# Kernel optimization log

Measured on AMD Instinct MI355X. Metric: run time of the kernel, lower is better.

## Reference

```python
import jax, jax.numpy as jnp
import numpy as np

B, L, D, H = 16, 512, 1024, 16
DH = D // H
NEG = -1e9  # stands in for -inf mask fill (same softmax result, grad-safe)


def setup_inputs() -> dict:
    key = jax.random.key(0)
    ks = jax.random.split(key, 8)
    x = jax.random.normal(ks[0], (B, L, D), dtype=jnp.float32)
    mask = jnp.ones((B, L), dtype=jnp.int64)
    qmask = jax.random.randint(ks[1], (B, L), 0, 9).astype(jnp.int64)
    # qkv_linear: Linear(D, 4D, bias=False); store as [D, 4D] so y = x @ Wqkv
    Wqkv = jax.random.normal(ks[2], (D, 4 * D), dtype=jnp.float32) / np.sqrt(D)
    # fc: Linear(D, D) with bias; store as [D, D] so y = x @ Wfc + bfc
    Wfc = jax.random.normal(ks[3], (D, D), dtype=jnp.float32) / np.sqrt(D)
    bfc = jnp.zeros((D,), dtype=jnp.float32)
    shift = jnp.abs(jax.random.normal(ks[4], (1,), dtype=jnp.float32)) + 0.001
    bias_p = -jnp.abs(jax.random.normal(ks[5], (1,), dtype=jnp.float32))
    return {"x": x, "mask": mask, "qmask": qmask, "Wqkv": Wqkv,
            "Wfc": Wfc, "bfc": bfc, "shift": shift, "bias_p": bias_p,
            "use_Gaussian": 1}


def reference(x, mask, qmask, Wqkv, Wfc, bfc, shift, bias_p, use_Gaussian):
    b, l, d = x.shape
    qkv = x @ Wqkv                                  # [B, L, 4D]
    q, k1, k2, v = jnp.split(qkv, 4, axis=-1)
    q = q.reshape(b, l, H, DH)                      # [B, L, H, dh]
    k1 = k1.reshape(b, l, H, DH)
    k2 = k2.reshape(b, l, H, DH)
    v = v.reshape(b, l, H, DH)

    attn_self = jnp.einsum('bqhd,bkhd->bhqk', q, k1)    # [B, H, L, L]
    attn_others = jnp.einsum('bqhd,bkhd->bhqk', q, k2)  # [B, H, L, L]

    same = (qmask[:, :, None] == qmask[:, None, :])[:, None]  # [B, 1, L, L]
    attn = jnp.where(same, attn_self, attn_others)  # scale == 1 (scale=False)

    key_valid = (mask != 0)[:, None, None, :]       # [B, 1, 1, L]
    attn = jnp.where(key_valid, attn, NEG)

    if use_Gaussian:
        idx = jnp.arange(l, dtype=jnp.float32)
        sq_dist = (idx[:, None] - idx[None, :]) ** 2        # [L, L]
        dis = -(shift[0] * sq_dist + bias_p[0])
        attn = attn + dis[None, None]

    attn = jax.nn.softmax(attn, axis=-1)            # dropout: eval mode (no-op)
    out = jnp.einsum('bhqk,bkhd->bqhd', attn, v).reshape(b, l, d)
    return out @ Wfc + bfc
```

## Files before the change

kernel.cpp:

```cpp
#include <hip/hip_runtime.h>
#include <hip/hip_bf16.h>

#define B_  16
#define L_  512
#define D_  1024
#define H_  16
#define DH_ 64
#define NEG_ (-1e9f)
#define QB_ 64
#define KB_ 64
#define LDP 72

#define GK  1024
#define NT  32

typedef unsigned short ushort_t;
typedef __attribute__((ext_vector_type(8))) short bf16x8;
typedef __attribute__((ext_vector_type(4))) float f32x4;

__device__ __forceinline__ ushort_t f2bf(float f) {
    unsigned u = __float_as_uint(f);
    u += 0x7FFFu + ((u >> 16) & 1u);
    return (ushort_t)(u >> 16);
}
__device__ __forceinline__ unsigned packbf(float a, float b) {
    return (unsigned)f2bf(a) | ((unsigned)f2bf(b) << 16);
}

__device__ __forceinline__ void gload_lds16(const void* g, void* l) {
    __builtin_amdgcn_global_load_lds(
        (const __attribute__((address_space(1))) void*)g,
        (__attribute__((address_space(3))) void*)l, 16, 0, 0);
}

__global__ __launch_bounds__(256) void conv_f32_bf16(const float* __restrict__ in,
                                                     ushort_t* __restrict__ out, int n) {
    const int i = (blockIdx.x * 256 + threadIdx.x) * 4;
    if (i < n) {
        const float4 v = *(const float4*)&in[i];
        ushort4 o;
        o.x = f2bf(v.x); o.y = f2bf(v.y); o.z = f2bf(v.z); o.w = f2bf(v.w);
        *(ushort4*)&out[i] = o;
    }
}

__global__ __launch_bounds__(256) void transpose_f32_bf16(const float* __restrict__ in,
                                                          ushort_t* __restrict__ out,
                                                          int R, int C) {
    __shared__ float tile[32][33];
    const int t  = threadIdx.x;
    const int r0 = blockIdx.y * 32, c0 = blockIdx.x * 32;
    const int tr = t >> 3;
    const int tc = (t & 7) * 4;
    const float4 v = *(const float4*)&in[(size_t)(r0 + tr) * C + c0 + tc];
    tile[tr][tc + 0] = v.x;
    tile[tr][tc + 1] = v.y;
    tile[tr][tc + 2] = v.z;
    tile[tr][tc + 3] = v.w;
    __syncthreads();
    ushort4 o;
    o.x = f2bf(tile[tc + 0][tr]);
    o.y = f2bf(tile[tc + 1][tr]);
    o.z = f2bf(tile[tc + 2][tr]);
    o.w = f2bf(tile[tc + 3][tr]);
    *(ushort4*)&out[(size_t)(c0 + tr) * R + r0 + tc] = o;
}

template <bool OUT_BF16>
__global__ __launch_bounds__(256) void gemm_bf16_mfma(const ushort_t* __restrict__ A,
                                                      const ushort_t* __restrict__ Bt,
                                                      const float* __restrict__ bias,
                                                      void* __restrict__ C,
                                                      int M, int N, int K) {
    __shared__ __align__(16) ushort_t As[128 * 64];
    __shared__ __align__(16) ushort_t Bs[128 * 64];

    const int t    = threadIdx.x;
    const int wave = t >> 6;
    const int lane = t & 63;
    const int m0   = blockIdx.y * 128;
    const int n0   = blockIdx.x * 128;
    const int wr   = wave >> 1;
    const int wc   = wave & 1;

    const int lrow = lane >> 3;
    const int lcol = (lane & 7) * 8;

    f32x4 acc[4][4] = {};

    for (int k0 = 0; k0 < K; k0 += 64) {
        #pragma unroll
        for (int i = 0; i < 4; ++i) {
            const int row = wave * 32 + i * 8;
            gload_lds16(A + (size_t)(m0 + row + lrow) * K + k0 + lcol,
                        As + (size_t)row * 64);
            gload_lds16(Bt + (size_t)(n0 + row + lrow) * K + k0 + lcol,
                        Bs + (size_t)row * 64);
        }
        __syncthreads();

        #pragma unroll
        for (int ks = 0; ks < 2; ++ks) {
            const int kb = ks * 32 + (lane >> 4) * 8;
            bf16x8 af[4], bfr[4];
            #pragma unroll
            for (int m = 0; m < 4; ++m)
                af[m] = *(const bf16x8*)&As[(wr * 64 + m * 16 + (lane & 15)) * 64 + kb];
            #pragma unroll
            for (int n = 0; n < 4; ++n)
                bfr[n] = *(const bf16x8*)&Bs[(wc * 64 + n * 16 + (lane & 15)) * 64 + kb];
            #pragma unroll
            for (int m = 0; m < 4; ++m)
                #pragma unroll
                for (int n = 0; n < 4; ++n)
                    acc[m][n] = __builtin_amdgcn_mfma_f32_16x16x32_bf16(
                        af[m], bfr[n], acc[m][n], 0, 0, 0);
        }
        __syncthreads();
    }

    #pragma unroll
    for (int m = 0; m < 4; ++m) {
        #pragma unroll
        for (int n = 0; n < 4; ++n) {
            const int col = n0 + wc * 64 + n * 16 + (lane & 15);
            const float bv = OUT_BF16 ? 0.f : bias[col];
            #pragma unroll
            for (int i = 0; i < 4; ++i) {
                const int row = m0 + wr * 64 + m * 16 + (lane >> 4) * 4 + i;
                const float v = acc[m][n][i];
                if (OUT_BF16)
                    ((ushort_t*)C)[(size_t)row * N + col] = f2bf(v);
                else
                    ((float*)C)[(size_t)row * N + col] = v + bv;
            }
        }
    }
}

__device__ __forceinline__ bf16x8 frag_ld(const ushort_t* tile, int row, int lhi) {
    const int slot = lhi ^ ((row >> 1) & 3);
    return *(const bf16x8*)&tile[row * 32 + (slot << 3)];
}

__global__ __launch_bounds__(512, 2) void gemm256_8p(const ushort_t* __restrict__ A,
                                                     const ushort_t* __restrict__ Bt,
                                                     ushort_t* __restrict__ C,
                                                     int nbn, int N) {
    extern __shared__ __align__(16) ushort_t lds[];

    const int t    = threadIdx.x;
    const int wave = t >> 6;
    const int lane = t & 63;
    const int wr   = wave >> 2;
    const int wc   = wave & 3;
    const int lhi  = lane >> 4;
    const int llo  = lane & 15;
    const int srow  = lane >> 2;
    const int sslot = (lane & 3) ^ ((lane >> 3) & 3);

    const int cpx = gridDim.x >> 3;
    const int bid = blockIdx.x;
    const int swz = (bid & 7) * cpx + (bid >> 3);
    const int m0  = (swz / nbn) * 256;
    const int n0  = (swz % nbn) * 256;

    #define STAGE_H(mat, gptr, grow0, kt, half)                                         \
        gload_lds16((gptr) + (size_t)((grow0) + (half) * 128 + (wave << 4) + srow) * GK \
                        + (kt) * 32 + (sslot << 3),                                     \
                    lds + ((((kt) & 3) * 2 + (mat)) * 8192                              \
                           + ((half) * 128 + (wave << 4)) * 32))

    f32x4 acc[8][4] = {};

    STAGE_H(0, A,  m0, 0, 0); STAGE_H(0, A,  m0, 0, 1);
    STAGE_H(1, Bt, n0, 0, 0); STAGE_H(1, Bt, n0, 0, 1);
    STAGE_H(0, A,  m0, 1, 0); STAGE_H(0, A,  m0, 1, 1);
    STAGE_H(1, Bt, n0, 1, 0); STAGE_H(1, Bt, n0, 1, 1);
    asm volatile("s_waitcnt vmcnt(4)" ::: "memory");
    __builtin_amdgcn_s_barrier();

    for (int kt = 0; kt < NT; ++kt) {
        const ushort_t* At  = lds + ((kt & 3) * 2 + 0) * 8192;
        const ushort_t* Bti = lds + ((kt & 3) * 2 + 1) * 8192;

        bf16x8 afr[4], bfr[4];

        #pragma unroll
        for (int n = 0; n < 4; ++n)
            bfr[n] = frag_ld(Bti, wc * 64 + n * 16 + llo, lhi);
        #pragma unroll
        for (int mi = 0; mi < 4; ++mi)
            afr[mi] = frag_ld(At, wr * 128 + mi * 16 + llo, lhi);
        if (kt + 2 < NT) {
            STAGE_H(0, A, m0, kt + 2, 0);
            STAGE_H(0, A, m0, kt + 2, 1);
        }
        __builtin_amdgcn_s_setprio(1);
        #pragma unroll
        for (int mi = 0; mi < 4; ++mi)
            #pragma unroll
            for (int n = 0; n < 4; ++n)
                acc[mi][n] = __builtin_amdgcn_mfma_f32_16x16x32_bf16(
                    afr[mi], bfr[n], acc[mi][n], 0, 0, 0);
        __builtin_amdgcn_s_setprio(0);

        #pragma unroll
        for (int mi = 0; mi < 4; ++mi)
            afr[mi] = frag_ld(At, wr * 128 + (mi + 4) * 16 + llo, lhi);
        if (kt + 2 < NT) {
            STAGE_H(1, Bt, n0, kt + 2, 0);
            STAGE_H(1, Bt, n0, kt + 2, 1);
        }
        __builtin_amdgcn_s_setprio(1);
        #pragma unroll
        for (int mi = 0; mi < 4; ++mi)
            #pragma unroll
            for (int n = 0; n < 4; ++n)
                acc[mi + 4][n] = __builtin_amdgcn_mfma_f32_16x16x32_bf16(
                    afr[mi], bfr[n], acc[mi + 4][n], 0, 0, 0);
        __builtin_amdgcn_s_setprio(0);

        if (kt + 2 < NT)      { asm volatile("s_waitcnt vmcnt(4)" ::: "memory"); }
        else if (kt + 1 < NT) { asm volatile("s_waitcnt vmcnt(0)" ::: "memory"); }
        __builtin_amdgcn_s_barrier();
    }
    #undef STAGE_H

    #pragma unroll
    for (int mi = 0; mi < 8; ++mi) {
        #pragma unroll
        for (int n = 0; n < 4; ++n) {
            const int col = n0 + wc * 64 + n * 16 + llo;
            #pragma unroll
            for (int i = 0; i < 4; ++i) {
                const int row = m0 + wr * 128 + mi * 16 + lhi * 4 + i;
                C[(size_t)row * N + col] = f2bf(acc[mi][n][i]);
            }
        }
    }
}

__global__ __launch_bounds__(256) void attn_mfma(const ushort_t* __restrict__ qkv,
                                                 const int* __restrict__ mask,
                                                 const int* __restrict__ qmask,
                                                 const float* __restrict__ shiftp,
                                                 const float* __restrict__ biasp,
                                                 const int* __restrict__ useg,
                                                 ushort_t* __restrict__ O) {
    __shared__ __align__(16) ushort_t K1s[KB_][LDP];
    __shared__ __align__(16) ushort_t K2s[KB_][LDP];
    __shared__ __align__(16) ushort_t Vt[DH_][LDP];
    __shared__ __align__(16) unsigned Ps32[QB_][36];
    __shared__ __align__(16) int      Ms[L_];

    const int t    = threadIdx.x;
    const int wave = t >> 6;
    const int lane = t & 63;
    const int lhi  = lane >> 4;
    const int llo  = lane & 15;

    const int orig = blockIdx.x;
    const int swz  = (orig & 7) * 256 + (orig >> 3);
    const int bh   = swz >> 3;
    const int qb   = swz & 7;
    const int b    = bh >> 4;
    const int h    = bh & 15;
    const int q0   = qb * QB_;

    const float shiftv = shiftp[0];
    const float biasv  = biasp[0];
    const int   useG   = useg[0];
    const size_t rowbase = (size_t)b * L_ * (4 * D_);
    const int    hoff    = h * DH_;

    {
        const int k = t;
        Ms[k]       = (qmask[b * L_ + k] << 1) | (mask[b * L_ + k] != 0 ? 1 : 0);
        Ms[k + 256] = (qmask[b * L_ + k + 256] << 1) | (mask[b * L_ + k + 256] != 0 ? 1 : 0);
    }

    const int gq = q0 + wave * 16 + llo;
    bf16x8 af_q[2];
    #pragma unroll
    for (int ks = 0; ks < 2; ++ks)
        af_q[ks] = *(const bf16x8*)&qkv[rowbase + (size_t)gq * (4 * D_) + hoff
                                        + ks * 32 + lhi * 8];
    const int qm_q = qmask[b * L_ + gq];

    int lo = 0, hi = (L_ / KB_) - 1;
    if (useG) {
        while (lo < hi) {
            const int k0 = lo * KB_;
            int dmin = (k0 > q0) ? (k0 - (q0 + KB_ - 1)) : (q0 - (k0 + KB_ - 1));
            if (dmin < 0) dmin = 0;
            if (shiftv * (float)dmin * (float)dmin > 240.f) ++lo; else break;
        }
        while (hi > lo) {
            const int k0 = hi * KB_;
            int dmin = (k0 > q0) ? (k0 - (q0 + KB_ - 1)) : (q0 - (k0 + KB_ - 1));
            if (dmin < 0) dmin = 0;
            if (shiftv * (float)dmin * (float)dmin > 240.f) --hi; else break;
        }
    }

    float m_run = -1e30f, l_run = 0.f;
    f32x4 acc_o[4] = {};

    const int srow8 = t >> 3;
    const int scol8 = (t & 7) * 8;
    const int vkv   = t & 63;
    const int vd0   = (t >> 6) * 8;

    uint4 pk1[2], pk2[2], pvv[2];

    #define ISSUE_KV(kt_) do {                                                          \
        const int k0_ = (kt_) * KB_;                                                    \
        _Pragma("unroll")                                                               \
        for (int it = 0; it < 2; ++it) {                                                \
            const int row = srow8 + it * 32;                                            \
            const size_t gb = rowbase + (size_t)(k0_ + row) * (4 * D_) + hoff + scol8;  \
            pk1[it] = *(const uint4*)&qkv[gb + D_];                                     \
            pk2[it] = *(const uint4*)&qkv[gb + 2 * D_];                                 \
            const int d_ = vd0 + it * 32;                                               \
            pvv[it] = *(const uint4*)&qkv[rowbase + (size_t)(k0_ + vkv) * (4 * D_)      \
                                          + 3 * D_ + hoff + d_];                        \
        }                                                                               \
    } while (0)

    ISSUE_KV(lo);

    for (int kt = lo; kt <= hi; ++kt) {
        const int k0 = kt * KB_;

        #pragma unroll
        for (int it = 0; it < 2; ++it) {
            const int row = srow8 + it * 32;
            *(uint4*)&K1s[row][scol8] = pk1[it];
            *(uint4*)&K2s[row][scol8] = pk2[it];
            const int d = vd0 + it * 32;
            const uint4 raw = pvv[it];
            Vt[d + 0][vkv] = (ushort_t)(raw.x & 0xFFFFu);
            Vt[d + 1][vkv] = (ushort_t)(raw.x >> 16);
            Vt[d + 2][vkv] = (ushort_t)(raw.y & 0xFFFFu);
            Vt[d + 3][vkv] = (ushort_t)(raw.y >> 16);
            Vt[d + 4][vkv] = (ushort_t)(raw.z & 0xFFFFu);
            Vt[d + 5][vkv] = (ushort_t)(raw.z >> 16);
            Vt[d + 6][vkv] = (ushort_t)(raw.w & 0xFFFFu);
            Vt[d + 7][vkv] = (ushort_t)(raw.w >> 16);
        }
        if (kt < hi) ISSUE_KV(kt + 1);
        __syncthreads();

        f32x4 s1[4], s2[4];
        #pragma unroll
        for (int n = 0; n < 4; ++n) { s1[n] = (f32x4){0,0,0,0}; s2[n] = (f32x4){0,0,0,0}; }
        #pragma unroll
        for (int ks = 0; ks < 2; ++ks) {
            const int kb = ks * 32 + lhi * 8;
            #pragma unroll
            for (int n = 0; n < 4; ++n) {
                const bf16x8 bk1 = *(const bf16x8*)&K1s[n * 16 + llo][kb];
                const bf16x8 bk2 = *(const bf16x8*)&K2s[n * 16 + llo][kb];
                s1[n] = __builtin_amdgcn_mfma_f32_16x16x32_bf16(bk1, af_q[ks], s1[n], 0, 0, 0);
                s2[n] = __builtin_amdgcn_mfma_f32_16x16x32_bf16(bk2, af_q[ks], s2[n], 0, 0, 0);
            }
        }

        float sv[4][4];
        float mx = -1e30f;
        #pragma unroll
        for (int n = 0; n < 4; ++n) {
            const int4 mc = *(const int4*)&Ms[k0 + n * 16 + lhi * 4];
            const int mci[4] = {mc.x, mc.y, mc.z, mc.w};
            #pragma unroll
            for (int i = 0; i < 4; ++i) {
                const int key = k0 + n * 16 + lhi * 4 + i;
                float x = ((mci[i] >> 1) == qm_q) ? s1[n][i] : s2[n][i];
                if (!(mci[i] & 1)) x = NEG_;
                if (useG) {
                    const float dq = (float)(gq - key);
                    x -= shiftv * dq * dq + biasv;
                }
                sv[n][i] = x;
                mx = fmaxf(mx, x);
            }
        }
        mx = fmaxf(mx, __shfl_xor(mx, 16));
        mx = fmaxf(mx, __shfl_xor(mx, 32));

        const float m_new = fmaxf(m_run, mx);
        const float scale = __expf(m_run - m_new);

        float p[4][4], ls = 0.f;
        #pragma unroll
        for (int n = 0; n < 4; ++n)
            #pragma unroll
            for (int i = 0; i < 4; ++i) {
                p[n][i] = __expf(sv[n][i] - m_new);
                ls += p[n][i];
            }
        ls += __shfl_xor(ls, 16);
        ls += __shfl_xor(ls, 32);
        l_run = l_run * scale + ls;
        m_run = m_new;

        #pragma unroll
        for (int n2 = 0; n2 < 4; ++n2) {
            acc_o[n2][0] *= scale; acc_o[n2][1] *= scale;
            acc_o[n2][2] *= scale; acc_o[n2][3] *= scale;
        }

        const int qrow = wave * 16 + llo;
        #pragma unroll
        for (int n = 0; n < 4; ++n) {
            uint2 w;
            w.x = packbf(p[n][0], p[n][1]);
            w.y = packbf(p[n][2], p[n][3]);
            *(uint2*)&Ps32[qrow][n * 8 + lhi * 2] = w;
        }

        #pragma unroll
        for (int ks = 0; ks < 2; ++ks) {
            const int kb = ks * 32 + lhi * 8;
            const bf16x8 bp = *(const bf16x8*)&Ps32[qrow][ks * 16 + lhi * 4];
            #pragma unroll
            for (int n2 = 0; n2 < 4; ++n2) {
                const bf16x8 av = *(const bf16x8*)&Vt[n2 * 16 + llo][kb];
                acc_o[n2] = __builtin_amdgcn_mfma_f32_16x16x32_bf16(av, bp, acc_o[n2], 0, 0, 0);
            }
        }
        __syncthreads();
    }
    #undef ISSUE_KV

    {
        const float inv = 1.f / l_run;
        const int qrow = wave * 16 + llo;
        #pragma unroll
        for (int n2 = 0; n2 < 4; ++n2) {
            uint2 w;
            w.x = packbf(acc_o[n2][0] * inv, acc_o[n2][1] * inv);
            w.y = packbf(acc_o[n2][2] * inv, acc_o[n2][3] * inv);
            *(uint2*)&Ps32[qrow][n2 * 8 + lhi * 2] = w;
        }
    }
    __syncthreads();
    {
        const int row = t >> 2;
        const int c4  = (t & 3) * 8;
        const uint4 a = *(const uint4*)&Ps32[row][c4];
        const uint4 b2 = *(const uint4*)&Ps32[row][c4 + 4];
        ushort_t* dst = &O[(size_t)(b * L_ + q0 + row) * D_ + hoff + c4 * 2];
        *(uint4*)dst       = a;
        *(uint4*)(dst + 8) = b2;
    }
}

extern "C" void kernel_launch(void* const* d_in, const int* in_sizes, int n_in,
                              void* d_out, int out_size, void* d_ws, size_t ws_size,
                              hipStream_t stream) {
    const float* x      = (const float*)d_in[0];
    const int*   mask   = (const int*)d_in[1];
    const int*   qmask  = (const int*)d_in[2];
    const float* Wqkv   = (const float*)d_in[3];
    const float* Wfc    = (const float*)d_in[4];
    const float* bfc    = (const float*)d_in[5];
    const float* shift  = (const float*)d_in[6];
    const float* bias_p = (const float*)d_in[7];
    const int*   useg   = (const int*)d_in[8];
    float*       out    = (float*)d_out;

    const int M  = B_ * L_;
    const int N1 = 4 * D_;

    ushort_t* qkv = (ushort_t*)d_ws;
    ushort_t* Obf = qkv + (size_t)M * N1;
    ushort_t* xbf = Obf + (size_t)M * D_;
    ushort_t* WqT = xbf + (size_t)M * D_;
    ushort_t* WfT = WqT + (size_t)N1 * D_;

    conv_f32_bf16<<<(M * D_) / 1024, 256, 0, stream>>>(x, xbf, M * D_);
    transpose_f32_bf16<<<dim3(N1 / 32, D_ / 32), 256, 0, stream>>>(Wqkv, WqT, D_, N1);
    transpose_f32_bf16<<<dim3(D_ / 32, D_ / 32), 256, 0, stream>>>(Wfc, WfT, D_, D_);

    gemm256_8p<<<dim3((M / 256) * (N1 / 256)), 512, 131072, stream>>>(
        xbf, WqT, qkv, N1 / 256, N1);

    attn_mfma<<<dim3((B_ * H_) * (L_ / QB_)), 256, 0, stream>>>(qkv, mask, qmask,
                                                                shift, bias_p, useg, Obf);

    gemm_bf16_mfma<false><<<dim3(D_ / 128, M / 128), 256, 0, stream>>>(
        Obf, WfT, bfc, out, M, D_, D_);
}
```

Before: 173.6 us.

## Fuse prep kernels, retile QKV GEMM to 128x256 with triple buffering, swizzle LDS

Merges the x conversion and both weight transposes into one launch, which cuts launch overhead. Replaces the 256x256, 4-stage QKV GEMM with a 128x256 tile that uses BK=64 and a 3-buffer pipeline, giving twice as many blocks for better CU fill. Adds an XOR swizzle to LDS staging in both GEMMs to reduce bank conflicts. In exchange, each block reuses less data and needs more LDS (147 KB per block), so occupancy may drop to one block per CU.

```diff
diff --git a/kernel.cpp b/kernel.cpp
--- a/kernel.cpp
+++ b/kernel.cpp
@@ -12,7 +12,7 @@
 #define LDP 72
 
 #define GK  1024
-#define NT  32
+#define NKT 16
 
 typedef unsigned short ushort_t;
 typedef __attribute__((ext_vector_type(8))) short bf16x8;
@@ -33,26 +33,36 @@
         (__attribute__((address_space(3))) void*)l, 16, 0, 0);
 }
 
-__global__ __launch_bounds__(256) void conv_f32_bf16(const float* __restrict__ in,
-                                                     ushort_t* __restrict__ out, int n) {
-    const int i = (blockIdx.x * 256 + threadIdx.x) * 4;
-    if (i < n) {
-        const float4 v = *(const float4*)&in[i];
+__global__ __launch_bounds__(256) void prep_all(const float* __restrict__ x,
+                                                const float* __restrict__ Wqkv,
+                                                const float* __restrict__ Wfc,
+                                                ushort_t* __restrict__ xbf,
+                                                ushort_t* __restrict__ WqT,
+                                                ushort_t* __restrict__ WfT) {
+    __shared__ float tile[32][33];
+    const int bid = blockIdx.x;
+    const int t   = threadIdx.x;
+
+    if (bid < 8192) {
+        const int i = (bid * 256 + t) * 4;
+        const float4 v = *(const float4*)&x[i];
         ushort4 o;
         o.x = f2bf(v.x); o.y = f2bf(v.y); o.z = f2bf(v.z); o.w = f2bf(v.w);
-        *(ushort4*)&out[i] = o;
-    }
-}
-
-__global__ __launch_bounds__(256) void transpose_f32_bf16(const float* __restrict__ in,
-                                                          ushort_t* __restrict__ out,
-                                                          int R, int C) {
-    __shared__ float tile[32][33];
-    const int t  = threadIdx.x;
-    const int r0 = blockIdx.y * 32, c0 = blockIdx.x * 32;
-    const int tr = t >> 3;
-    const int tc = (t & 7) * 4;
-    const float4 v = *(const float4*)&in[(size_t)(r0 + tr) * C + c0 + tc];
+        *(ushort4*)&xbf[i] = o;
+        return;
+    }
+    const float* src; ushort_t* dst; int C, gx, gy;
+    if (bid < 8192 + 4096) {
+        const int lb = bid - 8192;
+        src = Wqkv; dst = WqT; C = 4096; gx = lb & 127; gy = lb >> 7;
+    } else {
+        const int lb = bid - 12288;
+        src = Wfc;  dst = WfT; C = 1024; gx = lb & 31;  gy = lb >> 5;
+    }
+    const int R  = 1024;
+    const int r0 = gy * 32, c0 = gx * 32;
+    const int tr = t >> 3, tc = (t & 7) * 4;
+    const float4 v = *(const float4*)&src[(size_t)(r0 + tr) * C + c0 + tc];
     tile[tr][tc + 0] = v.x;
     tile[tr][tc + 1] = v.y;
     tile[tr][tc + 2] = v.z;
@@ -63,14 +73,13 @@
     o.y = f2bf(tile[tc + 1][tr]);
     o.z = f2bf(tile[tc + 2][tr]);
     o.w = f2bf(tile[tc + 3][tr]);
-    *(ushort4*)&out[(size_t)(c0 + tr) * R + r0 + tc] = o;
-}
-
-template <bool OUT_BF16>
+    *(ushort4*)&dst[(size_t)(c0 + tr) * R + r0 + tc] = o;
+}
+
 __global__ __launch_bounds__(256) void gemm_bf16_mfma(const ushort_t* __restrict__ A,
                                                       const ushort_t* __restrict__ Bt,
                                                       const float* __restrict__ bias,
-                                                      void* __restrict__ C,
+                                                      float* __restrict__ C,
                                                       int M, int N, int K) {
     __shared__ __align__(16) ushort_t As[128 * 64];
     __shared__ __align__(16) ushort_t Bs[128 * 64];
@@ -84,7 +93,9 @@
     const int wc   = wave & 1;
 
     const int lrow = lane >> 3;
-    const int lcol = (lane & 7) * 8;
+    const int ksl  = (lane & 7) ^ lrow;
+    const int llo  = lane & 15;
+    const int lhi  = lane >> 4;
 
     f32x4 acc[4][4] = {};
 
@@ -92,23 +103,26 @@
         #pragma unroll
         for (int i = 0; i < 4; ++i) {
             const int row = wave * 32 + i * 8;
-            gload_lds16(A + (size_t)(m0 + row + lrow) * K + k0 + lcol,
+            gload_lds16(A + (size_t)(m0 + row + lrow) * K + k0 + ksl * 8,
                         As + (size_t)row * 64);
-            gload_lds16(Bt + (size_t)(n0 + row + lrow) * K + k0 + lcol,
+            gload_lds16(Bt + (size_t)(n0 + row + lrow) * K + k0 + ksl * 8,
                         Bs + (size_t)row * 64);
         }
         __syncthreads();
 
         #pragma unroll
         for (int ks = 0; ks < 2; ++ks) {
-            const int kb = ks * 32 + (lane >> 4) * 8;
             bf16x8 af[4], bfr[4];
             #pragma unroll
-            for (int m = 0; m < 4; ++m)
-                af[m] = *(const bf16x8*)&As[(wr * 64 + m * 16 + (lane & 15)) * 64 + kb];
-            #pragma unroll
-            for (int n = 0; n < 4; ++n)
-                bfr[n] = *(const bf16x8*)&Bs[(wc * 64 + n * 16 + (lane & 15)) * 64 + kb];
+            for (int m = 0; m < 4; ++m) {
+                const int row = wr * 64 + m * 16 + llo;
+                af[m] = *(const bf16x8*)&As[row * 64 + (((ks * 4 + lhi) ^ (row & 7)) << 3)];
+            }
+            #pragma unroll
+            for (int n = 0; n < 4; ++n) {
+                const int row = wc * 64 + n * 16 + llo;
+                bfr[n] = *(const bf16x8*)&Bs[row * 64 + (((ks * 4 + lhi) ^ (row & 7)) << 3)];
+            }
             #pragma unroll
             for (int m = 0; m < 4; ++m)
                 #pragma unroll
@@ -123,30 +137,21 @@
     for (int m = 0; m < 4; ++m) {
         #pragma unroll
         for (int n = 0; n < 4; ++n) {
-            const int col = n0 + wc * 64 + n * 16 + (lane & 15);
-            const float bv = OUT_BF16 ? 0.f : bias[col];
+            const int col = n0 + wc * 64 + n * 16 + llo;
+            const float bv = bias[col];
             #pragma unroll
             for (int i = 0; i < 4; ++i) {
-                const int row = m0 + wr * 64 + m * 16 + (lane >> 4) * 4 + i;
-                const float v = acc[m][n][i];
-                if (OUT_BF16)
-                    ((ushort_t*)C)[(size_t)row * N + col] = f2bf(v);
-                else
-                    ((float*)C)[(size_t)row * N + col] = v + bv;
-            }
-        }
-    }
-}
-
-__device__ __forceinline__ bf16x8 frag_ld(const ushort_t* tile, int row, int lhi) {
-    const int slot = lhi ^ ((row >> 1) & 3);
-    return *(const bf16x8*)&tile[row * 32 + (slot << 3)];
-}
-
-__global__ __launch_bounds__(512, 2) void gemm256_8p(const ushort_t* __restrict__ A,
-                                                     const ushort_t* __restrict__ Bt,
-                                                     ushort_t* __restrict__ C,
-                                                     int nbn, int N) {
+                const int row = m0 + wr * 64 + m * 16 + lhi * 4 + i;
+                C[(size_t)row * N + col] = acc[m][n][i] + bv;
+            }
+        }
+    }
+}
+
+__global__ __launch_bounds__(512, 2) void gemm128x256(const ushort_t* __restrict__ A,
+                                                      const ushort_t* __restrict__ Bt,
+                                                      ushort_t* __restrict__ C,
+                                                      int nbn, int N) {
     extern __shared__ __align__(16) ushort_t lds[];
 
     const int t    = threadIdx.x;
@@ -156,85 +161,84 @@
     const int wc   = wave & 3;
     const int lhi  = lane >> 4;
     const int llo  = lane & 15;
-    const int srow  = lane >> 2;
-    const int sslot = (lane & 3) ^ ((lane >> 3) & 3);
 
     const int cpx = gridDim.x >> 3;
-    const int bid = blockIdx.x;
-    const int swz = (bid & 7) * cpx + (bid >> 3);
-    const int m0  = (swz / nbn) * 256;
+    const int swz = (blockIdx.x & 7) * cpx + (blockIdx.x >> 3);
+    const int m0  = (swz / nbn) * 128;
     const int n0  = (swz % nbn) * 256;
 
-    #define STAGE_H(mat, gptr, grow0, kt, half)                                         \
-        gload_lds16((gptr) + (size_t)((grow0) + (half) * 128 + (wave << 4) + srow) * GK \
-                        + (kt) * 32 + (sslot << 3),                                     \
-                    lds + ((((kt) & 3) * 2 + (mat)) * 8192                              \
-                           + ((half) * 128 + (wave << 4)) * 32))
-
-    f32x4 acc[8][4] = {};
-
-    STAGE_H(0, A,  m0, 0, 0); STAGE_H(0, A,  m0, 0, 1);
-    STAGE_H(1, Bt, n0, 0, 0); STAGE_H(1, Bt, n0, 0, 1);
-    STAGE_H(0, A,  m0, 1, 0); STAGE_H(0, A,  m0, 1, 1);
-    STAGE_H(1, Bt, n0, 1, 0); STAGE_H(1, Bt, n0, 1, 1);
-    asm volatile("s_waitcnt vmcnt(4)" ::: "memory");
+    #define STAGE_A(buf, kt)                                                     \
+        _Pragma("unroll")                                                        \
+        for (int j = 0; j < 2; ++j) {                                            \
+            const int row_ = (j * 512 + t) >> 3;                                 \
+            const int ks_  = (t & 7) ^ (row_ & 7);                               \
+            gload_lds16(A + (size_t)(m0 + row_) * GK + (kt) * 64 + ks_ * 8,      \
+                        lds + (buf) * 24576 + j * 4096 + (t >> 6) * 512);        \
+        }
+    #define STAGE_B(buf, kt)                                                     \
+        _Pragma("unroll")                                                        \
+        for (int j = 0; j < 4; ++j) {                                            \
+            const int row_ = (j * 512 + t) >> 3;                                 \
+            const int ks_  = (t & 7) ^ (row_ & 7);                               \
+            gload_lds16(Bt + (size_t)(n0 + row_) * GK + (kt) * 64 + ks_ * 8,     \
+                        lds + (buf) * 24576 + 8192 + j * 4096 + (t >> 6) * 512); \
+        }
+
+    f32x4 acc[4][4] = {};
+
+    STAGE_A(0, 0); STAGE_B(0, 0);
+    STAGE_A(1, 1); STAGE_B(1, 1);
+    asm volatile("s_waitcnt vmcnt(6)" ::: "memory");
     __builtin_amdgcn_s_barrier();
 
-    for (int kt = 0; kt < NT; ++kt) {
-        const ushort_t* At  = lds + ((kt & 3) * 2 + 0) * 8192;
-        const ushort_t* Bti = lds + ((kt & 3) * 2 + 1) * 8192;
-
-        bf16x8 afr[4], bfr[4];
-
+    for (int kt = 0; kt < NKT; ++kt) {
+        const ushort_t* Ab = lds + (kt % 3) * 24576;
+        const ushort_t* Bb = Ab + 8192;
+
+        bf16x8 afr[4][2], bfr[4][2];
+        #pragma unroll
+        for (int mi = 0; mi < 4; ++mi)
+            #pragma unroll
+            for (int kk = 0; kk < 2; ++kk) {
+                const int row = wr * 64 + mi * 16 + llo;
+                afr[mi][kk] = *(const bf16x8*)&Ab[row * 64 + (((kk * 4 + lhi) ^ (row & 7)) << 3)];
+            }
         #pragma unroll
         for (int n = 0; n < 4; ++n)
-            bfr[n] = frag_ld(Bti, wc * 64 + n * 16 + llo, lhi);
-        #pragma unroll
-        for (int mi = 0; mi < 4; ++mi)
-            afr[mi] = frag_ld(At, wr * 128 + mi * 16 + llo, lhi);
-        if (kt + 2 < NT) {
-            STAGE_H(0, A, m0, kt + 2, 0);
-            STAGE_H(0, A, m0, kt + 2, 1);
-        }
+            #pragma unroll
+            for (int kk = 0; kk < 2; ++kk) {
+                const int row = wc * 64 + n * 16 + llo;
+                bfr[n][kk] = *(const bf16x8*)&Bb[row * 64 + (((kk * 4 + lhi) ^ (row & 7)) << 3)];
+            }
+
+        if (kt + 2 < NKT) { STAGE_A((kt + 2) % 3, kt + 2); STAGE_B((kt + 2) % 3, kt + 2); }
+
         __builtin_amdgcn_s_setprio(1);
         #pragma unroll
-        for (int mi = 0; mi < 4; ++mi)
-            #pragma unroll
-            for (int n = 0; n < 4; ++n)
-                acc[mi][n] = __builtin_amdgcn_mfma_f32_16x16x32_bf16(
-                    afr[mi], bfr[n], acc[mi][n], 0, 0, 0);
+        for (int kk = 0; kk < 2; ++kk)
+            #pragma unroll
+            for (int mi = 0; mi < 4; ++mi)
+                #pragma unroll
+                for (int n = 0; n < 4; ++n)
+                    acc[mi][n] = __builtin_amdgcn_mfma_f32_16x16x32_bf16(
+                        afr[mi][kk], bfr[n][kk], acc[mi][n], 0, 0, 0);
         __builtin_amdgcn_s_setprio(0);
 
-        #pragma unroll
-        for (int mi = 0; mi < 4; ++mi)
-            afr[mi] = frag_ld(At, wr * 128 + (mi + 4) * 16 + llo, lhi);
-        if (kt + 2 < NT) {
-            STAGE_H(1, Bt, n0, kt + 2, 0);
-            STAGE_H(1, Bt, n0, kt + 2, 1);
-        }
-        __builtin_amdgcn_s_setprio(1);
-        #pragma unroll
-        for (int mi = 0; mi < 4; ++mi)
-            #pragma unroll
-            for (int n = 0; n < 4; ++n)
-                acc[mi + 4][n] = __builtin_amdgcn_mfma_f32_16x16x32_bf16(
-                    afr[mi], bfr[n], acc[mi + 4][n], 0, 0, 0);
-        __builtin_amdgcn_s_setprio(0);
-
-        if (kt + 2 < NT)      { asm volatile("s_waitcnt vmcnt(4)" ::: "memory"); }
-        else if (kt + 1 < NT) { asm volatile("s_waitcnt vmcnt(0)" ::: "memory"); }
+        if (kt + 2 < NKT)      { asm volatile("s_waitcnt vmcnt(6)" ::: "memory"); }
+        else if (kt + 1 < NKT) { asm volatile("s_waitcnt vmcnt(0)" ::: "memory"); }
         __builtin_amdgcn_s_barrier();
     }
-    #undef STAGE_H
+    #undef STAGE_A
+    #undef STAGE_B
 
     #pragma unroll
-    for (int mi = 0; mi < 8; ++mi) {
+    for (int mi = 0; mi < 4; ++mi) {
         #pragma unroll
         for (int n = 0; n < 4; ++n) {
             const int col = n0 + wc * 64 + n * 16 + llo;
             #pragma unroll
             for (int i = 0; i < 4; ++i) {
-                const int row = m0 + wr * 128 + mi * 16 + lhi * 4 + i;
+                const int row = m0 + wr * 64 + mi * 16 + lhi * 4 + i;
                 C[(size_t)row * N + col] = f2bf(acc[mi][n][i]);
             }
         }
@@ -480,16 +484,14 @@
     ushort_t* WqT = xbf + (size_t)M * D_;
     ushort_t* WfT = WqT + (size_t)N1 * D_;
 
-    conv_f32_bf16<<<(M * D_) / 1024, 256, 0, stream>>>(x, xbf, M * D_);
-    transpose_f32_bf16<<<dim3(N1 / 32, D_ / 32), 256, 0, stream>>>(Wqkv, WqT, D_, N1);
-    transpose_f32_bf16<<<dim3(D_ / 32, D_ / 32), 256, 0, stream>>>(Wfc, WfT, D_, D_);
-
-    gemm256_8p<<<dim3((M / 256) * (N1 / 256)), 512, 131072, stream>>>(
-        xbf, WqT, qkv, N1 / 256, N1);
+    prep_all<<<dim3(8192 + 4096 + 1024), 256, 0, stream>>>(x, Wqkv, Wfc,
+                                                           xbf, WqT, WfT);
+
+    gemm128x256<<<dim3(1024), 512, 147456, stream>>>(xbf, WqT, qkv, N1 / 256, N1);
 
     attn_mfma<<<dim3((B_ * H_) * (L_ / QB_)), 256, 0, stream>>>(qkv, mask, qmask,
                                                                 shift, bias_p, useg, Obf);
 
-    gemm_bf16_mfma<false><<<dim3(D_ / 128, M / 128), 256, 0, stream>>>(
+    gemm_bf16_mfma<<<dim3(D_ / 128, M / 128), 256, 0, stream>>>(
         Obf, WfT, bfc, out, M, D_, D_);
 }
```

Measured after the change: 176.2 us. No clear change (+1.5%).

## Shrink attention tiles, fuse prep kernels, swizzle LDS in output GEMM

Applied to the files above, without the earlier changes.

Attention now uses 32x32 query/key tiles with 128-thread blocks, so the Gaussian-distance band culling skips more far-away key tiles and more blocks run. The three fp32-to-bf16 conversion and transpose kernels are merged into one launch to cut launch overhead. The output projection GEMM XOR-swizzles its LDS layout to reduce bank conflicts. Smaller attention tiles lower operand reuse per tile and raise the per-tile synchronisation overhead.

```diff
diff --git a/kernel.cpp b/kernel.cpp
--- a/kernel.cpp
+++ b/kernel.cpp
@@ -7,8 +7,8 @@
 #define H_  16
 #define DH_ 64
 #define NEG_ (-1e9f)
-#define QB_ 64
-#define KB_ 64
+#define QB2 32
+#define KB2 32
 #define LDP 72
 
 #define GK  1024
@@ -33,26 +33,36 @@
         (__attribute__((address_space(3))) void*)l, 16, 0, 0);
 }
 
-__global__ __launch_bounds__(256) void conv_f32_bf16(const float* __restrict__ in,
-                                                     ushort_t* __restrict__ out, int n) {
-    const int i = (blockIdx.x * 256 + threadIdx.x) * 4;
-    if (i < n) {
-        const float4 v = *(const float4*)&in[i];
+__global__ __launch_bounds__(256) void prep_all(const float* __restrict__ x,
+                                                const float* __restrict__ Wqkv,
+                                                const float* __restrict__ Wfc,
+                                                ushort_t* __restrict__ xbf,
+                                                ushort_t* __restrict__ WqT,
+                                                ushort_t* __restrict__ WfT) {
+    __shared__ float tile[32][33];
+    const int bid = blockIdx.x;
+    const int t   = threadIdx.x;
+
+    if (bid < 8192) {
+        const int i = (bid * 256 + t) * 4;
+        const float4 v = *(const float4*)&x[i];
         ushort4 o;
         o.x = f2bf(v.x); o.y = f2bf(v.y); o.z = f2bf(v.z); o.w = f2bf(v.w);
-        *(ushort4*)&out[i] = o;
-    }
-}
-
-__global__ __launch_bounds__(256) void transpose_f32_bf16(const float* __restrict__ in,
-                                                          ushort_t* __restrict__ out,
-                                                          int R, int C) {
-    __shared__ float tile[32][33];
-    const int t  = threadIdx.x;
-    const int r0 = blockIdx.y * 32, c0 = blockIdx.x * 32;
-    const int tr = t >> 3;
-    const int tc = (t & 7) * 4;
-    const float4 v = *(const float4*)&in[(size_t)(r0 + tr) * C + c0 + tc];
+        *(ushort4*)&xbf[i] = o;
+        return;
+    }
+    const float* src; ushort_t* dst; int C, gx, gy;
+    if (bid < 8192 + 4096) {
+        const int lb = bid - 8192;
+        src = Wqkv; dst = WqT; C = 4096; gx = lb & 127; gy = lb >> 7;
+    } else {
+        const int lb = bid - 12288;
+        src = Wfc;  dst = WfT; C = 1024; gx = lb & 31;  gy = lb >> 5;
+    }
+    const int R  = 1024;
+    const int r0 = gy * 32, c0 = gx * 32;
+    const int tr = t >> 3, tc = (t & 7) * 4;
+    const float4 v = *(const float4*)&src[(size_t)(r0 + tr) * C + c0 + tc];
     tile[tr][tc + 0] = v.x;
     tile[tr][tc + 1] = v.y;
     tile[tr][tc + 2] = v.z;
@@ -63,14 +73,13 @@
     o.y = f2bf(tile[tc + 1][tr]);
     o.z = f2bf(tile[tc + 2][tr]);
     o.w = f2bf(tile[tc + 3][tr]);
-    *(ushort4*)&out[(size_t)(c0 + tr) * R + r0 + tc] = o;
-}
-
-template <bool OUT_BF16>
+    *(ushort4*)&dst[(size_t)(c0 + tr) * R + r0 + tc] = o;
+}
+
 __global__ __launch_bounds__(256) void gemm_bf16_mfma(const ushort_t* __restrict__ A,
                                                       const ushort_t* __restrict__ Bt,
                                                       const float* __restrict__ bias,
-                                                      void* __restrict__ C,
+                                                      float* __restrict__ C,
                                                       int M, int N, int K) {
     __shared__ __align__(16) ushort_t As[128 * 64];
     __shared__ __align__(16) ushort_t Bs[128 * 64];
@@ -84,7 +93,9 @@
     const int wc   = wave & 1;
 
     const int lrow = lane >> 3;
-    const int lcol = (lane & 7) * 8;
+    const int ksl  = (lane & 7) ^ lrow;
+    const int llo  = lane & 15;
+    const int lhi  = lane >> 4;
 
     f32x4 acc[4][4] = {};
 
@@ -92,23 +103,26 @@
         #pragma unroll
         for (int i = 0; i < 4; ++i) {
             const int row = wave * 32 + i * 8;
-            gload_lds16(A + (size_t)(m0 + row + lrow) * K + k0 + lcol,
+            gload_lds16(A + (size_t)(m0 + row + lrow) * K + k0 + ksl * 8,
                         As + (size_t)row * 64);
-            gload_lds16(Bt + (size_t)(n0 + row + lrow) * K + k0 + lcol,
+            gload_lds16(Bt + (size_t)(n0 + row + lrow) * K + k0 + ksl * 8,
                         Bs + (size_t)row * 64);
         }
         __syncthreads();
 
         #pragma unroll
         for (int ks = 0; ks < 2; ++ks) {
-            const int kb = ks * 32 + (lane >> 4) * 8;
             bf16x8 af[4], bfr[4];
             #pragma unroll
-            for (int m = 0; m < 4; ++m)
-                af[m] = *(const bf16x8*)&As[(wr * 64 + m * 16 + (lane & 15)) * 64 + kb];
-            #pragma unroll
-            for (int n = 0; n < 4; ++n)
-                bfr[n] = *(const bf16x8*)&Bs[(wc * 64 + n * 16 + (lane & 15)) * 64 + kb];
+            for (int m = 0; m < 4; ++m) {
+                const int row = wr * 64 + m * 16 + llo;
+                af[m] = *(const bf16x8*)&As[row * 64 + (((ks * 4 + lhi) ^ (row & 7)) << 3)];
+            }
+            #pragma unroll
+            for (int n = 0; n < 4; ++n) {
+                const int row = wc * 64 + n * 16 + llo;
+                bfr[n] = *(const bf16x8*)&Bs[row * 64 + (((ks * 4 + lhi) ^ (row & 7)) << 3)];
+            }
             #pragma unroll
             for (int m = 0; m < 4; ++m)
                 #pragma unroll
@@ -123,16 +137,12 @@
     for (int m = 0; m < 4; ++m) {
         #pragma unroll
         for (int n = 0; n < 4; ++n) {
-            const int col = n0 + wc * 64 + n * 16 + (lane & 15);
-            const float bv = OUT_BF16 ? 0.f : bias[col];
+            const int col = n0 + wc * 64 + n * 16 + llo;
+            const float bv = bias[col];
             #pragma unroll
             for (int i = 0; i < 4; ++i) {
-                const int row = m0 + wr * 64 + m * 16 + (lane >> 4) * 4 + i;
-                const float v = acc[m][n][i];
-                if (OUT_BF16)
-                    ((ushort_t*)C)[(size_t)row * N + col] = f2bf(v);
-                else
-                    ((float*)C)[(size_t)row * N + col] = v + bv;
+                const int row = m0 + wr * 64 + m * 16 + lhi * 4 + i;
+                C[(size_t)row * N + col] = acc[m][n][i] + bv;
             }
         }
     }
@@ -160,8 +170,7 @@
     const int sslot = (lane & 3) ^ ((lane >> 3) & 3);
 
     const int cpx = gridDim.x >> 3;
-    const int bid = blockIdx.x;
-    const int swz = (bid & 7) * cpx + (bid >> 3);
+    const int swz = (blockIdx.x & 7) * cpx + (blockIdx.x >> 3);
     const int m0  = (swz / nbn) * 256;
     const int n0  = (swz % nbn) * 256;
 
@@ -241,17 +250,17 @@
     }
 }
 
-__global__ __launch_bounds__(256) void attn_mfma(const ushort_t* __restrict__ qkv,
+__global__ __launch_bounds__(128) void attn_mfma(const ushort_t* __restrict__ qkv,
                                                  const int* __restrict__ mask,
                                                  const int* __restrict__ qmask,
                                                  const float* __restrict__ shiftp,
                                                  const float* __restrict__ biasp,
                                                  const int* __restrict__ useg,
                                                  ushort_t* __restrict__ O) {
-    __shared__ __align__(16) ushort_t K1s[KB_][LDP];
-    __shared__ __align__(16) ushort_t K2s[KB_][LDP];
-    __shared__ __align__(16) ushort_t Vt[DH_][LDP];
-    __shared__ __align__(16) unsigned Ps32[QB_][36];
+    __shared__ __align__(16) ushort_t K1s[KB2][LDP];
+    __shared__ __align__(16) ushort_t K2s[KB2][LDP];
+    __shared__ __align__(16) ushort_t Vt[DH_][36];
+    __shared__ __align__(16) unsigned Ps32[QB2][36];
     __shared__ __align__(16) int      Ms[L_];
 
     const int t    = threadIdx.x;
@@ -261,12 +270,12 @@
     const int llo  = lane & 15;
 
     const int orig = blockIdx.x;
-    const int swz  = (orig & 7) * 256 + (orig >> 3);
-    const int bh   = swz >> 3;
-    const int qb   = swz & 7;
+    const int swz  = (orig & 7) * 512 + (orig >> 3);
+    const int bh   = swz >> 4;
+    const int qb   = swz & 15;
     const int b    = bh >> 4;
     const int h    = bh & 15;
-    const int q0   = qb * QB_;
+    const int q0   = qb * QB2;
 
     const float shiftv = shiftp[0];
     const float biasv  = biasp[0];
@@ -274,10 +283,10 @@
     const size_t rowbase = (size_t)b * L_ * (4 * D_);
     const int    hoff    = h * DH_;
 
-    {
-        const int k = t;
-        Ms[k]       = (qmask[b * L_ + k] << 1) | (mask[b * L_ + k] != 0 ? 1 : 0);
-        Ms[k + 256] = (qmask[b * L_ + k + 256] << 1) | (mask[b * L_ + k + 256] != 0 ? 1 : 0);
+    #pragma unroll
+    for (int j = 0; j < 4; ++j) {
+        const int k = t + j * 128;
+        Ms[k] = (qmask[b * L_ + k] << 1) | (mask[b * L_ + k] != 0 ? 1 : 0);
     }
 
     const int gq = q0 + wave * 16 + llo;
@@ -288,17 +297,17 @@
                                         + ks * 32 + lhi * 8];
     const int qm_q = qmask[b * L_ + gq];
 
-    int lo = 0, hi = (L_ / KB_) - 1;
+    int lo = 0, hi = (L_ / KB2) - 1;
     if (useG) {
         while (lo < hi) {
-            const int k0 = lo * KB_;
-            int dmin = (k0 > q0) ? (k0 - (q0 + KB_ - 1)) : (q0 - (k0 + KB_ - 1));
+            const int k0 = lo * KB2;
+            int dmin = (k0 > q0) ? (k0 - (q0 + QB2 - 1)) : (q0 - (k0 + KB2 - 1));
             if (dmin < 0) dmin = 0;
             if (shiftv * (float)dmin * (float)dmin > 240.f) ++lo; else break;
         }
         while (hi > lo) {
-            const int k0 = hi * KB_;
-            int dmin = (k0 > q0) ? (k0 - (q0 + KB_ - 1)) : (q0 - (k0 + KB_ - 1));
+            const int k0 = hi * KB2;
+            int dmin = (k0 > q0) ? (k0 - (q0 + QB2 - 1)) : (q0 - (k0 + KB2 - 1));
             if (dmin < 0) dmin = 0;
             if (shiftv * (float)dmin * (float)dmin > 240.f) --hi; else break;
         }
@@ -307,37 +316,35 @@
     float m_run = -1e30f, l_run = 0.f;
     f32x4 acc_o[4] = {};
 
-    const int srow8 = t >> 3;
-    const int scol8 = (t & 7) * 8;
-    const int vkv   = t & 63;
-    const int vd0   = (t >> 6) * 8;
+    const int srow = t >> 2;
+    const int scol = (t & 3) * 8;
+    const int vkv  = t & 31;
+    const int vd0  = (t >> 5) * 8;
 
     uint4 pk1[2], pk2[2], pvv[2];
 
     #define ISSUE_KV(kt_) do {                                                          \
-        const int k0_ = (kt_) * KB_;                                                    \
+        const int k0_ = (kt_) * KB2;                                                    \
         _Pragma("unroll")                                                               \
         for (int it = 0; it < 2; ++it) {                                                \
-            const int row = srow8 + it * 32;                                            \
-            const size_t gb = rowbase + (size_t)(k0_ + row) * (4 * D_) + hoff + scol8;  \
+            const size_t gb = rowbase + (size_t)(k0_ + srow) * (4 * D_) + hoff          \
+                              + scol + it * 32;                                         \
             pk1[it] = *(const uint4*)&qkv[gb + D_];                                     \
             pk2[it] = *(const uint4*)&qkv[gb + 2 * D_];                                 \
-            const int d_ = vd0 + it * 32;                                               \
             pvv[it] = *(const uint4*)&qkv[rowbase + (size_t)(k0_ + vkv) * (4 * D_)      \
-                                          + 3 * D_ + hoff + d_];                        \
+                                          + 3 * D_ + hoff + vd0 + it * 32];             \
         }                                                                               \
     } while (0)
 
     ISSUE_KV(lo);
 
     for (int kt = lo; kt <= hi; ++kt) {
-        const int k0 = kt * KB_;
+        const int k0 = kt * KB2;
 
         #pragma unroll
         for (int it = 0; it < 2; ++it) {
-            const int row = srow8 + it * 32;
-            *(uint4*)&K1s[row][scol8] = pk1[it];
-            *(uint4*)&K2s[row][scol8] = pk2[it];
+            *(uint4*)&K1s[srow][scol + it * 32] = pk1[it];
+            *(uint4*)&K2s[srow][scol + it * 32] = pk2[it];
             const int d = vd0 + it * 32;
             const uint4 raw = pvv[it];
             Vt[d + 0][vkv] = (ushort_t)(raw.x & 0xFFFFu);
@@ -352,14 +359,14 @@
         if (kt < hi) ISSUE_KV(kt + 1);
         __syncthreads();
 
-        f32x4 s1[4], s2[4];
-        #pragma unroll
-        for (int n = 0; n < 4; ++n) { s1[n] = (f32x4){0,0,0,0}; s2[n] = (f32x4){0,0,0,0}; }
+        f32x4 s1[2], s2[2];
+        #pragma unroll
+        for (int n = 0; n < 2; ++n) { s1[n] = (f32x4){0,0,0,0}; s2[n] = (f32x4){0,0,0,0}; }
         #pragma unroll
         for (int ks = 0; ks < 2; ++ks) {
             const int kb = ks * 32 + lhi * 8;
             #pragma unroll
-            for (int n = 0; n < 4; ++n) {
+            for (int n = 0; n < 2; ++n) {
                 const bf16x8 bk1 = *(const bf16x8*)&K1s[n * 16 + llo][kb];
                 const bf16x8 bk2 = *(const bf16x8*)&K2s[n * 16 + llo][kb];
                 s1[n] = __builtin_amdgcn_mfma_f32_16x16x32_bf16(bk1, af_q[ks], s1[n], 0, 0, 0);
@@ -367,10 +374,10 @@
             }
         }
 
-        float sv[4][4];
+        float sv[2][4];
         float mx = -1e30f;
         #pragma unroll
-        for (int n = 0; n < 4; ++n) {
+        for (int n = 0; n < 2; ++n) {
             const int4 mc = *(const int4*)&Ms[k0 + n * 16 + lhi * 4];
             const int mci[4] = {mc.x, mc.y, mc.z, mc.w};
             #pragma unroll
@@ -392,9 +399,9 @@
         const float m_new = fmaxf(m_run, mx);
         const float scale = __expf(m_run - m_new);
 
-        float p[4][4], ls = 0.f;
-        #pragma unroll
-        for (int n = 0; n < 4; ++n)
+        float p[2][4], ls = 0.f;
+        #pragma unroll
+        for (int n = 0; n < 2; ++n)
             #pragma unroll
             for (int i = 0; i < 4; ++i) {
                 p[n][i] = __expf(sv[n][i] - m_new);
@@ -413,17 +420,16 @@
 
         const int qrow = wave * 16 + llo;
         #pragma unroll
-        for (int n = 0; n < 4; ++n) {
+        for (int n = 0; n < 2; ++n) {
             uint2 w;
             w.x = packbf(p[n][0], p[n][1]);
             w.y = packbf(p[n][2], p[n][3]);
             *(uint2*)&Ps32[qrow][n * 8 + lhi * 2] = w;
         }
 
-        #pragma unroll
-        for (int ks = 0; ks < 2; ++ks) {
-            const int kb = ks * 32 + lhi * 8;
-            const bf16x8 bp = *(const bf16x8*)&Ps32[qrow][ks * 16 + lhi * 4];
+        {
+            const int kb = lhi * 8;
+            const bf16x8 bp = *(const bf16x8*)&Ps32[qrow][lhi * 4];
             #pragma unroll
             for (int n2 = 0; n2 < 4; ++n2) {
                 const bf16x8 av = *(const bf16x8*)&Vt[n2 * 16 + llo][kb];
@@ -449,7 +455,7 @@
     {
         const int row = t >> 2;
         const int c4  = (t & 3) * 8;
-        const uint4 a = *(const uint4*)&Ps32[row][c4];
+        const uint4 a  = *(const uint4*)&Ps32[row][c4];
         const uint4 b2 = *(const uint4*)&Ps32[row][c4 + 4];
         ushort_t* dst = &O[(size_t)(b * L_ + q0 + row) * D_ + hoff + c4 * 2];
         *(uint4*)dst       = a;
@@ -480,16 +486,15 @@
     ushort_t* WqT = xbf + (size_t)M * D_;
     ushort_t* WfT = WqT + (size_t)N1 * D_;
 
-    conv_f32_bf16<<<(M * D_) / 1024, 256, 0, stream>>>(x, xbf, M * D_);
-    transpose_f32_bf16<<<dim3(N1 / 32, D_ / 32), 256, 0, stream>>>(Wqkv, WqT, D_, N1);
-    transpose_f32_bf16<<<dim3(D_ / 32, D_ / 32), 256, 0, stream>>>(Wfc, WfT, D_, D_);
+    prep_all<<<dim3(8192 + 4096 + 1024), 256, 0, stream>>>(x, Wqkv, Wfc,
+                                                           xbf, WqT, WfT);
 
     gemm256_8p<<<dim3((M / 256) * (N1 / 256)), 512, 131072, stream>>>(
         xbf, WqT, qkv, N1 / 256, N1);
 
-    attn_mfma<<<dim3((B_ * H_) * (L_ / QB_)), 256, 0, stream>>>(qkv, mask, qmask,
+    attn_mfma<<<dim3((B_ * H_) * (L_ / QB2)), 128, 0, stream>>>(qkv, mask, qmask,
                                                                 shift, bias_p, useg, Obf);
 
-    gemm_bf16_mfma<false><<<dim3(D_ / 128, M / 128), 256, 0, stream>>>(
+    gemm_bf16_mfma<<<dim3(D_ / 128, M / 128), 256, 0, stream>>>(
         Obf, WfT, bfc, out, M, D_, D_);
 }
```

New measurement: 159.6 us. 1.09x faster.
